# Performance work log

Measured on AMD Instinct MI355X. Metric: run time of the kernel, lower is better.

## Reference

```python
import jax, jax.numpy as jnp
import numpy as np

N_NODES = 100000


def gcn_conv(x, edge_index, W, b, n_nodes):
    """PyG GCNConv: add self-loops, symmetric deg norm, linear, scatter-add, bias."""
    self_loops = jnp.arange(n_nodes, dtype=edge_index.dtype)
    src = jnp.concatenate([edge_index[0], self_loops])  # [E+N]
    dst = jnp.concatenate([edge_index[1], self_loops])  # [E+N]
    xw = x @ W  # [N, out]
    deg = jax.ops.segment_sum(jnp.ones_like(dst, dtype=xw.dtype), dst, num_segments=n_nodes)
    deg_inv_sqrt = jnp.where(deg > 0, jax.lax.rsqrt(deg), 0.0)
    norm = deg_inv_sqrt[src] * deg_inv_sqrt[dst]  # [E+N]
    msg = xw[src] * norm[:, None]                 # [E+N, out]
    out = jax.ops.segment_sum(msg, dst, num_segments=n_nodes)
    return out + b


def setup_inputs() -> dict:
    key = jax.random.key(0)
    ks = jax.random.split(key, 8)
    n, e, d_in, h = N_NODES, 3200000, 128, 16
    x = jax.random.normal(ks[0], (n, d_in), dtype=jnp.float32)
    edge_index = jax.random.randint(ks[1], (2, e), 0, n, dtype=jnp.int64)
    W1 = jax.random.normal(ks[2], (d_in, h), dtype=jnp.float32) / np.sqrt(d_in)
    b1 = jnp.zeros((h,), dtype=jnp.float32)
    W2 = jax.random.normal(ks[3], (h, h), dtype=jnp.float32) / np.sqrt(h)
    b2 = jnp.zeros((h,), dtype=jnp.float32)
    W_lin = jax.random.normal(ks[4], (h, 1), dtype=jnp.float32) / np.sqrt(h)
    b_lin = jnp.zeros((1,), dtype=jnp.float32)
    return {"x": x, "edge_index": edge_index, "W1": W1, "b1": b1,
            "W2": W2, "b2": b2, "W_lin": W_lin, "b_lin": b_lin}


def reference(x, edge_index, W1, b1, W2, b2, W_lin, b_lin):
    n = x.shape[0]
    h = gcn_conv(x, edge_index, W1, b1, n)
    h = jax.nn.relu(h)
    # dropout is identity in eval mode (training=False)
    h = gcn_conv(h, edge_index, W2, b2, n)
    h = jax.nn.relu(h)
    out = h @ W_lin + b_lin  # [N, 1]
    return out.squeeze(-1)   # [N]
```

## Files before the change

### kernel.cpp

```cpp
#include <hip/hip_runtime.h>
#include <hip/hip_fp16.h>

#define DIN 128
#define HDIM 16
#define NB 512
#define BDIV_MAX 256
#define CAPB 7168
#define HSTR 17
#define BIN_EPT 16
#define TPB 512
#define BINSZ (TPB * BIN_EPT)
#define FXS 65536.0f
#define FXI (1.0f / 65536.0f)

__device__ __forceinline__ float4 f4add(float4 a, float4 b) {
    return make_float4(a.x + b.x, a.y + b.y, a.z + b.z, a.w + b.w);
}

__device__ __forceinline__ float4 h4_to_f4(uint2 u) {
    __half2 a = *(__half2*)&u.x, b = *(__half2*)&u.y;
    float2 fa = __half22float2(a), fb = __half22float2(b);
    return make_float4(fa.x, fa.y, fb.x, fb.y);
}
__device__ __forceinline__ uint2 f4_to_h4(float4 v) {
    __half2 a = __floats2half2_rn(v.x, v.y);
    __half2 b = __floats2half2_rn(v.z, v.w);
    uint2 u;
    u.x = *(unsigned*)&a;
    u.y = *(unsigned*)&b;
    return u;
}

__device__ __forceinline__ int load_idx(const void* ei, long long i, int is64) {
    return is64 ? (int)((const long long*)ei)[i] : ((const int*)ei)[i];
}

__device__ __forceinline__ void fx_acc(int* a, float4 v) {
    atomicAdd(a + 0, __float2int_rn(v.x * FXS));
    atomicAdd(a + 1, __float2int_rn(v.y * FXS));
    atomicAdd(a + 2, __float2int_rn(v.z * FXS));
    atomicAdd(a + 3, __float2int_rn(v.w * FXS));
}

__global__ __launch_bounds__(512) void k_main(const void* __restrict__ ei, long long E,
                                              int bdiv, unsigned Mdiv,
                                              int* __restrict__ bcur,
                                              unsigned int* __restrict__ recs,
                                              const float* __restrict__ x,
                                              const float* __restrict__ W1,
                                              unsigned int* __restrict__ y1,
                                              int n, int nbin) {
    __shared__ int cnt[NB];
    __shared__ int base[NB];
    __shared__ float Ws[DIN * HDIM];
    int tid = threadIdx.x;
    if ((int)blockIdx.x < nbin) {
        unsigned probe = ((const unsigned*)ei)[1 + 2 * (tid & 63)];
        int is64 = (__ballot(probe != 0) == 0ull) ? 1 : 0;
        cnt[tid] = 0;
        __syncthreads();
        long long e0 = (long long)blockIdx.x * BINSZ;
        int s[BIN_EPT], dl[BIN_EPT], b[BIN_EPT];
        if (e0 + BINSZ <= E) {
            int d[BIN_EPT];
            if (is64) {
                const longlong2* ps = (const longlong2*)((const long long*)ei + e0);
                const longlong2* pd = (const longlong2*)((const long long*)ei + E + e0);
#pragma unroll
                for (int i = 0; i < BIN_EPT / 2; i++) {
                    longlong2 vs = ps[i * TPB + tid];
                    longlong2 vd = pd[i * TPB + tid];
                    s[2 * i + 0] = (int)vs.x; s[2 * i + 1] = (int)vs.y;
                    d[2 * i + 0] = (int)vd.x; d[2 * i + 1] = (int)vd.y;
                }
            } else {
                const int4* ps = (const int4*)((const int*)ei + e0);
                const int4* pd = (const int4*)((const int*)ei + E + e0);
#pragma unroll
                for (int i = 0; i < BIN_EPT / 4; i++) {
                    int4 vs = ps[i * TPB + tid];
                    int4 vd = pd[i * TPB + tid];
                    s[4 * i + 0] = vs.x; s[4 * i + 1] = vs.y;
                    s[4 * i + 2] = vs.z; s[4 * i + 3] = vs.w;
                    d[4 * i + 0] = vd.x; d[4 * i + 1] = vd.y;
                    d[4 * i + 2] = vd.z; d[4 * i + 3] = vd.w;
                }
            }
#pragma unroll
            for (int i = 0; i < BIN_EPT; i++) {
                int bb = Mdiv ? (int)__umulhi((unsigned)d[i], Mdiv) : d[i];
                b[i] = bb;
                dl[i] = d[i] - bb * bdiv;
                atomicAdd(&cnt[bb], 1);
            }
        } else {
#pragma unroll
            for (int i = 0; i < BIN_EPT; i++) {
                long long e = e0 + (long long)i * TPB + tid;
                if (e < E) {
                    s[i] = load_idx(ei, e, is64);
                    int d = load_idx(ei, E + e, is64);
                    int bb = Mdiv ? (int)__umulhi((unsigned)d, Mdiv) : d;
                    b[i] = bb;
                    dl[i] = d - bb * bdiv;
                    atomicAdd(&cnt[bb], 1);
                } else {
                    b[i] = -1;
                }
            }
        }
        __syncthreads();
        base[tid] = atomicAdd(&bcur[tid], cnt[tid]);
        cnt[tid] = 0;
        __syncthreads();
#pragma unroll
        for (int i = 0; i < BIN_EPT; i++) {
            if (b[i] >= 0) {
                int off = atomicAdd(&cnt[b[i]], 1);
                int pos = base[b[i]] + off;
                if (pos < CAPB) {
                    recs[(size_t)b[i] * CAPB + pos] =
                        ((unsigned)dl[i] << 18) | (unsigned)s[i];
                }
            }
        }
    } else {
        for (int i = tid; i < DIN * HDIM; i += TPB) Ws[i] = W1[i];
        __syncthreads();
        int node = ((int)blockIdx.x - nbin) * TPB + tid;
        if (node >= n) return;
        uint2* yr = (uint2*)(y1 + (size_t)node * 8);
        float acc[HDIM];
#pragma unroll
        for (int f = 0; f < HDIM; f++) acc[f] = 0.f;
        const float4* xr = (const float4*)(x + (size_t)node * DIN);
#pragma unroll 8
        for (int k4 = 0; k4 < DIN / 4; k4++) {
            float4 xv = xr[k4];
            int k = k4 * 4;
#pragma unroll
            for (int f = 0; f < HDIM; f++) {
                acc[f] += xv.x * Ws[(k + 0) * HDIM + f];
                acc[f] += xv.y * Ws[(k + 1) * HDIM + f];
                acc[f] += xv.z * Ws[(k + 2) * HDIM + f];
                acc[f] += xv.w * Ws[(k + 3) * HDIM + f];
            }
        }
#pragma unroll
        for (int q = 0; q < 4; q++)
            yr[q] = f4_to_h4(make_float4(acc[q * 4 + 0], acc[q * 4 + 1],
                                         acc[q * 4 + 2], acc[q * 4 + 3]));
    }
}

__global__ __launch_bounds__(512) void k_deg(const unsigned int* __restrict__ recs,
                                             const int* __restrict__ bcur,
                                             float* __restrict__ dis,
                                             unsigned int* __restrict__ y1,
                                             int n, int bdiv) {
    __shared__ int cnt[BDIV_MAX];
    int tid = threadIdx.x, b = blockIdx.x;
    if (tid < BDIV_MAX) cnt[tid] = 0;
    __syncthreads();
    int lo = b * bdiv; if (lo > n) lo = n;
    int hi = lo + bdiv; if (hi > n) hi = n;
    int nd = hi - lo;
    int m = bcur[b]; if (m > CAPB) m = CAPB;
    const unsigned int* r = recs + (size_t)b * CAPB;
    for (int i = tid; i < m; i += 512)
        atomicAdd(&cnt[r[i] >> 18], 1);
    __syncthreads();
    int q = tid & 3, g = tid >> 2;
    uint2* yv = (uint2*)y1;
    for (int j = g; j < nd; j += 128) {
        int node = lo + j;
        float dv = rsqrtf((float)cnt[j] + 1.0f);
        if (q == 0) dis[node] = dv;
        float4 t = h4_to_f4(yv[(size_t)node * 4 + q]);
        yv[(size_t)node * 4 + q] =
            f4_to_h4(make_float4(t.x * dv, t.y * dv, t.z * dv, t.w * dv));
    }
}

__global__ __launch_bounds__(512) void k_agg1(const unsigned int* __restrict__ recs,
                                              const int* __restrict__ bcur,
                                              const float* __restrict__ dis,
                                              const unsigned int* __restrict__ y1,
                                              const float* __restrict__ b1,
                                              const float* __restrict__ W2,
                                              unsigned int* __restrict__ y2,
                                              int n, int bdiv) {
    __shared__ int acc[BDIV_MAX * HSTR];
    __shared__ unsigned int sh[CAPB];
    __shared__ float4 Ws4[HDIM][4];
    int tid = threadIdx.x, b = blockIdx.x;
    if (tid < HDIM * 4)
        ((float4*)Ws4)[tid] = ((const float4*)W2)[tid];
    int lo = b * bdiv; if (lo > n) lo = n;
    int hi = lo + bdiv; if (hi > n) hi = n;
    int nd = hi - lo;
    for (int i = tid; i < bdiv * HSTR; i += 512) acc[i] = 0;
    int m = bcur[b]; if (m > CAPB) m = CAPB;
    const uint4* r4 = (const uint4*)(recs + (size_t)b * CAPB);
    int m4 = (m + 3) >> 2;
    for (int k = tid; k < m4; k += 512) ((uint4*)sh)[k] = r4[k];
    __syncthreads();
    const uint2* yv = (const uint2*)y1;
    int q = tid & 3, g = tid >> 2;
    int i = g;
    for (; i + 384 < m; i += 512) {
        unsigned r0 = sh[i], r1 = sh[i + 128], r2 = sh[i + 256], r3 = sh[i + 384];
        float4 v0 = h4_to_f4(yv[(size_t)(r0 & 0x3FFFFu) * 4 + q]);
        float4 v1 = h4_to_f4(yv[(size_t)(r1 & 0x3FFFFu) * 4 + q]);
        float4 v2 = h4_to_f4(yv[(size_t)(r2 & 0x3FFFFu) * 4 + q]);
        float4 v3 = h4_to_f4(yv[(size_t)(r3 & 0x3FFFFu) * 4 + q]);
        fx_acc(&acc[(r0 >> 18) * HSTR + q * 4], v0);
        fx_acc(&acc[(r1 >> 18) * HSTR + q * 4], v1);
        fx_acc(&acc[(r2 >> 18) * HSTR + q * 4], v2);
        fx_acc(&acc[(r3 >> 18) * HSTR + q * 4], v3);
    }
    for (; i < m; i += 128) {
        unsigned r0 = sh[i];
        float4 v0 = h4_to_f4(yv[(size_t)(r0 & 0x3FFFFu) * 4 + q]);
        fx_acc(&acc[(r0 >> 18) * HSTR + q * 4], v0);
    }
    __syncthreads();
    float4 bb = ((const float4*)b1)[q];
    for (int j = g; j < nd; j += 128) {
        int node = lo + j;
        float dv = dis[node];
        int* ap = &acc[j * HSTR + q * 4];
        float4 a = make_float4((float)ap[0] * FXI, (float)ap[1] * FXI,
                               (float)ap[2] * FXI, (float)ap[3] * FXI);
        a = f4add(a, h4_to_f4(yv[(size_t)node * 4 + q]));
        float4 h;
        h.x = fmaxf(dv * a.x + bb.x, 0.f);
        h.y = fmaxf(dv * a.y + bb.y, 0.f);
        h.z = fmaxf(dv * a.z + bb.z, 0.f);
        h.w = fmaxf(dv * a.w + bb.w, 0.f);
        float4 o = make_float4(0.f, 0.f, 0.f, 0.f);
#pragma unroll
        for (int k = 0; k < 4; k++) {
            float4 hk;
            hk.x = __shfl(h.x, k, 4); hk.y = __shfl(h.y, k, 4);
            hk.z = __shfl(h.z, k, 4); hk.w = __shfl(h.w, k, 4);
            float hv[4] = {hk.x, hk.y, hk.z, hk.w};
#pragma unroll
            for (int c = 0; c < 4; c++) {
                float4 w = Ws4[k * 4 + c][q];
                o.x += hv[c] * w.x; o.y += hv[c] * w.y;
                o.z += hv[c] * w.z; o.w += hv[c] * w.w;
            }
        }
        ((uint2*)y2)[(size_t)node * 4 + q] =
            f4_to_h4(make_float4(o.x * dv, o.y * dv, o.z * dv, o.w * dv));
    }
}

__global__ __launch_bounds__(512) void k_agg2(const unsigned int* __restrict__ recs,
                                              const int* __restrict__ bcur,
                                              const float* __restrict__ dis,
                                              const unsigned int* __restrict__ y2,
                                              const float* __restrict__ b2,
                                              const float* __restrict__ Wlin,
                                              const float* __restrict__ blin,
                                              float* __restrict__ out,
                                              int n, int bdiv) {
    __shared__ int acc[BDIV_MAX * HSTR];
    __shared__ unsigned int sh[CAPB];
    int tid = threadIdx.x, b = blockIdx.x;
    int lo = b * bdiv; if (lo > n) lo = n;
    int hi = lo + bdiv; if (hi > n) hi = n;
    int nd = hi - lo;
    for (int i = tid; i < bdiv * HSTR; i += 512) acc[i] = 0;
    int m = bcur[b]; if (m > CAPB) m = CAPB;
    const uint4* r4 = (const uint4*)(recs + (size_t)b * CAPB);
    int m4 = (m + 3) >> 2;
    for (int k = tid; k < m4; k += 512) ((uint4*)sh)[k] = r4[k];
    __syncthreads();
    const uint2* yv = (const uint2*)y2;
    int q = tid & 3, g = tid >> 2;
    int i = g;
    for (; i + 384 < m; i += 512) {
        unsigned r0 = sh[i], r1 = sh[i + 128], r2 = sh[i + 256], r3 = sh[i + 384];
        float4 v0 = h4_to_f4(yv[(size_t)(r0 & 0x3FFFFu) * 4 + q]);
        float4 v1 = h4_to_f4(yv[(size_t)(r1 & 0x3FFFFu) * 4 + q]);
        float4 v2 = h4_to_f4(yv[(size_t)(r2 & 0x3FFFFu) * 4 + q]);
        float4 v3 = h4_to_f4(yv[(size_t)(r3 & 0x3FFFFu) * 4 + q]);
        fx_acc(&acc[(r0 >> 18) * HSTR + q * 4], v0);
        fx_acc(&acc[(r1 >> 18) * HSTR + q * 4], v1);
        fx_acc(&acc[(r2 >> 18) * HSTR + q * 4], v2);
        fx_acc(&acc[(r3 >> 18) * HSTR + q * 4], v3);
    }
    for (; i < m; i += 128) {
        unsigned r0 = sh[i];
        float4 v0 = h4_to_f4(yv[(size_t)(r0 & 0x3FFFFu) * 4 + q]);
        fx_acc(&acc[(r0 >> 18) * HSTR + q * 4], v0);
    }
    __syncthreads();
    float4 bb = ((const float4*)b2)[q];
    float4 wl = ((const float4*)Wlin)[q];
    for (int j = g; j < nd; j += 128) {
        int node = lo + j;
        float dv = dis[node];
        int* ap = &acc[j * HSTR + q * 4];
        float4 a = make_float4((float)ap[0] * FXI, (float)ap[1] * FXI,
                               (float)ap[2] * FXI, (float)ap[3] * FXI);
        a = f4add(a, h4_to_f4(yv[(size_t)node * 4 + q]));
        float v = 0.f;
        v += fmaxf(dv * a.x + bb.x, 0.f) * wl.x;
        v += fmaxf(dv * a.y + bb.y, 0.f) * wl.y;
        v += fmaxf(dv * a.z + bb.z, 0.f) * wl.z;
        v += fmaxf(dv * a.w + bb.w, 0.f) * wl.w;
        v += __shfl_xor(v, 1, 4);
        v += __shfl_xor(v, 2, 4);
        if (q == 0) out[node] = v + blin[0];
    }
}

extern "C" void kernel_launch(void* const* d_in, const int* in_sizes, int n_in,
                              void* d_out, int out_size, void* d_ws, size_t ws_size,
                              hipStream_t stream) {
    const float* x    = (const float*)d_in[0];
    const void*  ei   = d_in[1];
    const float* W1   = (const float*)d_in[2];
    const float* b1   = (const float*)d_in[3];
    const float* W2   = (const float*)d_in[4];
    const float* b2   = (const float*)d_in[5];
    const float* Wlin = (const float*)d_in[6];
    const float* blin = (const float*)d_in[7];
    float* out = (float*)d_out;

    const int n = in_sizes[0] / DIN;
    const long long E = in_sizes[1] / 2;
    const int bdiv = (n + NB - 1) / NB;
    const unsigned Mdiv = (bdiv > 1)
        ? (unsigned)(((1ull << 32) + (unsigned)bdiv - 1) / (unsigned)bdiv) : 0u;

    char* ws = (char*)d_ws;
    size_t off = 0;
    auto alloc = [&](size_t bytes) { char* p = ws + off; off += (bytes + 255) & ~(size_t)255; return p; };
    int*   bcur = (int*)alloc(NB * 4);
    float* dis  = (float*)alloc((size_t)n * 4);
    unsigned int* y1 = (unsigned int*)alloc((size_t)n * 8 * 4);
    unsigned int* y2 = (unsigned int*)alloc((size_t)n * 8 * 4);
    unsigned int* recs = (unsigned int*)alloc((size_t)NB * CAPB * 4);

    const int nb_xw  = (n + TPB - 1) / TPB;
    const int nb_bin = (int)((E + BINSZ - 1) / BINSZ);

    hipMemsetAsync(bcur, 0, NB * sizeof(int), stream);
    k_main<<<nb_bin + nb_xw, TPB, 0, stream>>>(ei, E, bdiv, Mdiv, bcur, recs, x, W1, y1, n, nb_bin);
    k_deg<<<NB, 512, 0, stream>>>(recs, bcur, dis, y1, n, bdiv);
    k_agg1<<<NB, 512, 0, stream>>>(recs, bcur, dis, y1, b1, W2, y2, n, bdiv);
    k_agg2<<<NB, 512, 0, stream>>>(recs, bcur, dis, y2, b2, Wlin, blin, out, n, bdiv);
}
```

Before: 184.9 us.

## Replace shared-memory atomic scatter with per-block counting sort and register gather

Both aggregation kernels now counting-sort each bin's edge records by destination inside shared memory, padding every node's list to a multiple of four with a dummy zero row at index n. Each node then gathers its neighbours' half-precision features into registers, with no fixed-point LDS atomics. This targets the cost of four integer atomics per edge per thread. In exchange it adds a 512-wide prefix scan, a second pass over the records, a padding fill, and an extra zeroed feature row. Degree is recomputed from the sorted counts, so the precomputed dis array is no longer read.

After: 194.7 us. 1.05x slower.

```diff
diff --git a/kernel.cpp b/kernel.cpp
--- a/kernel.cpp
+++ b/kernel.cpp
@@ -6,12 +6,10 @@
 #define NB 512
 #define BDIV_MAX 256
 #define CAPB 7168
-#define HSTR 17
+#define CAPP 7936
 #define BIN_EPT 16
 #define TPB 512
 #define BINSZ (TPB * BIN_EPT)
-#define FXS 65536.0f
-#define FXI (1.0f / 65536.0f)
 
 __device__ __forceinline__ float4 f4add(float4 a, float4 b) {
     return make_float4(a.x + b.x, a.y + b.y, a.z + b.z, a.w + b.w);
@@ -33,13 +31,6 @@
 
 __device__ __forceinline__ int load_idx(const void* ei, long long i, int is64) {
     return is64 ? (int)((const long long*)ei)[i] : ((const int*)ei)[i];
-}
-
-__device__ __forceinline__ void fx_acc(int* a, float4 v) {
-    atomicAdd(a + 0, __float2int_rn(v.x * FXS));
-    atomicAdd(a + 1, __float2int_rn(v.y * FXS));
-    atomicAdd(a + 2, __float2int_rn(v.z * FXS));
-    atomicAdd(a + 3, __float2int_rn(v.w * FXS));
 }
 
 __global__ __launch_bounds__(512) void k_main(const void* __restrict__ ei, long long E,
@@ -128,8 +119,14 @@
         for (int i = tid; i < DIN * HDIM; i += TPB) Ws[i] = W1[i];
         __syncthreads();
         int node = ((int)blockIdx.x - nbin) * TPB + tid;
-        if (node >= n) return;
+        if (node > n) return;
         uint2* yr = (uint2*)(y1 + (size_t)node * 8);
+        if (node == n) {
+            uint2 z; z.x = 0u; z.y = 0u;
+#pragma unroll
+            for (int q = 0; q < 4; q++) yr[q] = z;
+            return;
+        }
         float acc[HDIM];
 #pragma unroll
         for (int f = 0; f < HDIM; f++) acc[f] = 0.f;
@@ -182,72 +179,107 @@
     }
 }
 
-__global__ __launch_bounds__(512) void k_agg1(const unsigned int* __restrict__ recs,
-                                              const int* __restrict__ bcur,
-                                              const float* __restrict__ dis,
-                                              const unsigned int* __restrict__ y1,
-                                              const float* __restrict__ b1,
-                                              const float* __restrict__ W2,
-                                              unsigned int* __restrict__ y2,
-                                              int n, int bdiv) {
-    __shared__ int acc[BDIV_MAX * HSTR];
-    __shared__ unsigned int sh[CAPB];
+__global__ __launch_bounds__(512) void k_sg1(const unsigned int* __restrict__ recs,
+                                             const int* __restrict__ bcur,
+                                             const unsigned int* __restrict__ y1,
+                                             const float* __restrict__ b1,
+                                             const float* __restrict__ W2,
+                                             unsigned int* __restrict__ y2,
+                                             int n, int bdiv) {
+    __shared__ int cnt_sh[BDIV_MAX];
+    __shared__ int sc[512];
+    __shared__ int stx[BDIV_MAX];
+    __shared__ int dgx[BDIV_MAX];
+    __shared__ unsigned int ord[CAPP];
     __shared__ float4 Ws4[HDIM][4];
     int tid = threadIdx.x, b = blockIdx.x;
     if (tid < HDIM * 4)
         ((float4*)Ws4)[tid] = ((const float4*)W2)[tid];
+    if (b == 0 && tid < 4) {
+        uint2 z; z.x = 0u; z.y = 0u;
+        ((uint2*)y2)[(size_t)n * 4 + tid] = z;
+    }
     int lo = b * bdiv; if (lo > n) lo = n;
     int hi = lo + bdiv; if (hi > n) hi = n;
     int nd = hi - lo;
-    for (int i = tid; i < bdiv * HSTR; i += 512) acc[i] = 0;
+    if (tid < BDIV_MAX) cnt_sh[tid] = 0;
+    __syncthreads();
     int m = bcur[b]; if (m > CAPB) m = CAPB;
-    const uint4* r4 = (const uint4*)(recs + (size_t)b * CAPB);
-    int m4 = (m + 3) >> 2;
-    for (int k = tid; k < m4; k += 512) ((uint4*)sh)[k] = r4[k];
-    __syncthreads();
+    const unsigned int* r = recs + (size_t)b * CAPB;
+    for (int i = tid; i < m; i += 512)
+        atomicAdd(&cnt_sh[r[i] >> 18], 1);
+    __syncthreads();
+    int v  = (tid < nd) ? cnt_sh[tid] : 0;
+    int pv = (v + 3) & ~3;
+    sc[tid] = pv;
+    __syncthreads();
+    for (int off = 1; off < 512; off <<= 1) {
+        int t = (tid >= off) ? sc[tid - off] : 0;
+        __syncthreads();
+        sc[tid] += t;
+        __syncthreads();
+    }
+    int ptot = sc[511];
+    if (ptot > CAPP) ptot = CAPP;
+    if (tid < nd) {
+        int excl = sc[tid] - pv;
+        stx[tid] = excl; dgx[tid] = v;
+        cnt_sh[tid] = excl;
+    }
+    for (int i = tid; i < ptot; i += 512) ord[i] = (unsigned)n;
+    __syncthreads();
+    for (int i = tid; i < m; i += 512) {
+        unsigned rv = r[i];
+        int pos = atomicAdd(&cnt_sh[rv >> 18], 1);
+        if (pos < CAPP) ord[pos] = rv & 0x3FFFFu;
+    }
+    __syncthreads();
+    int q = tid & 3, g = tid >> 2;
     const uint2* yv = (const uint2*)y1;
-    int q = tid & 3, g = tid >> 2;
-    int i = g;
-    for (; i + 384 < m; i += 512) {
-        unsigned r0 = sh[i], r1 = sh[i + 128], r2 = sh[i + 256], r3 = sh[i + 384];
-        float4 v0 = h4_to_f4(yv[(size_t)(r0 & 0x3FFFFu) * 4 + q]);
-        float4 v1 = h4_to_f4(yv[(size_t)(r1 & 0x3FFFFu) * 4 + q]);
-        float4 v2 = h4_to_f4(yv[(size_t)(r2 & 0x3FFFFu) * 4 + q]);
-        float4 v3 = h4_to_f4(yv[(size_t)(r3 & 0x3FFFFu) * 4 + q]);
-        fx_acc(&acc[(r0 >> 18) * HSTR + q * 4], v0);
-        fx_acc(&acc[(r1 >> 18) * HSTR + q * 4], v1);
-        fx_acc(&acc[(r2 >> 18) * HSTR + q * 4], v2);
-        fx_acc(&acc[(r3 >> 18) * HSTR + q * 4], v3);
-    }
-    for (; i < m; i += 128) {
-        unsigned r0 = sh[i];
-        float4 v0 = h4_to_f4(yv[(size_t)(r0 & 0x3FFFFu) * 4 + q]);
-        fx_acc(&acc[(r0 >> 18) * HSTR + q * 4], v0);
-    }
-    __syncthreads();
     float4 bb = ((const float4*)b1)[q];
     for (int j = g; j < nd; j += 128) {
         int node = lo + j;
-        float dv = dis[node];
-        int* ap = &acc[j * HSTR + q * 4];
-        float4 a = make_float4((float)ap[0] * FXI, (float)ap[1] * FXI,
-                               (float)ap[2] * FXI, (float)ap[3] * FXI);
-        a = f4add(a, h4_to_f4(yv[(size_t)node * 4 + q]));
+        int st = stx[j], dg = dgx[j];
+        int pe = st + ((dg + 3) & ~3);
+        float4 a0 = make_float4(0.f, 0.f, 0.f, 0.f), a1 = a0, a2 = a0, a3 = a0;
+        int k = st;
+        for (; k + 8 <= pe; k += 8) {
+            int4 c0 = *(const int4*)&ord[k];
+            int4 c1 = *(const int4*)&ord[k + 4];
+            uint2 v0 = yv[(size_t)c0.x * 4 + q], v1 = yv[(size_t)c0.y * 4 + q];
+            uint2 v2 = yv[(size_t)c0.z * 4 + q], v3 = yv[(size_t)c0.w * 4 + q];
+            uint2 v4 = yv[(size_t)c1.x * 4 + q], v5 = yv[(size_t)c1.y * 4 + q];
+            uint2 v6 = yv[(size_t)c1.z * 4 + q], v7 = yv[(size_t)c1.w * 4 + q];
+            a0 = f4add(a0, h4_to_f4(v0)); a1 = f4add(a1, h4_to_f4(v1));
+            a2 = f4add(a2, h4_to_f4(v2)); a3 = f4add(a3, h4_to_f4(v3));
+            a0 = f4add(a0, h4_to_f4(v4)); a1 = f4add(a1, h4_to_f4(v5));
+            a2 = f4add(a2, h4_to_f4(v6)); a3 = f4add(a3, h4_to_f4(v7));
+        }
+        for (; k < pe; k += 4) {
+            int4 c0 = *(const int4*)&ord[k];
+            uint2 v0 = yv[(size_t)c0.x * 4 + q], v1 = yv[(size_t)c0.y * 4 + q];
+            uint2 v2 = yv[(size_t)c0.z * 4 + q], v3 = yv[(size_t)c0.w * 4 + q];
+            a0 = f4add(a0, h4_to_f4(v0)); a1 = f4add(a1, h4_to_f4(v1));
+            a2 = f4add(a2, h4_to_f4(v2)); a3 = f4add(a3, h4_to_f4(v3));
+        }
+        float4 acc = f4add(f4add(a0, a1), f4add(a2, a3));
+        acc = f4add(acc, h4_to_f4(yv[(size_t)node * 4 + q]));
+        float dv = rsqrtf((float)dg + 1.0f);
         float4 h;
-        h.x = fmaxf(dv * a.x + bb.x, 0.f);
-        h.y = fmaxf(dv * a.y + bb.y, 0.f);
-        h.z = fmaxf(dv * a.z + bb.z, 0.f);
-        h.w = fmaxf(dv * a.w + bb.w, 0.f);
+        h.x = fmaxf(dv * acc.x + bb.x, 0.f);
+        h.y = fmaxf(dv * acc.y + bb.y, 0.f);
+        h.z = fmaxf(dv * acc.z + bb.z, 0.f);
+        h.w = fmaxf(dv * acc.w + bb.w, 0.f);
         float4 o = make_float4(0.f, 0.f, 0.f, 0.f);
 #pragma unroll
-        for (int k = 0; k < 4; k++) {
+        for (int kk = 0; kk < 4; kk++) {
             float4 hk;
-            hk.x = __shfl(h.x, k, 4); hk.y = __shfl(h.y, k, 4);
-            hk.z = __shfl(h.z, k, 4); hk.w = __shfl(h.w, k, 4);
+            hk.x = __shfl(h.x, kk, 4); hk.y = __shfl(h.y, kk, 4);
+            hk.z = __shfl(h.z, kk, 4); hk.w = __shfl(h.w, kk, 4);
             float hv[4] = {hk.x, hk.y, hk.z, hk.w};
 #pragma unroll
             for (int c = 0; c < 4; c++) {
-                float4 w = Ws4[k * 4 + c][q];
+                float4 w = Ws4[kk * 4 + c][q];
                 o.x += hv[c] * w.x; o.y += hv[c] * w.y;
                 o.z += hv[c] * w.z; o.w += hv[c] * w.w;
             }
@@ -257,64 +289,95 @@
     }
 }
 
-__global__ __launch_bounds__(512) void k_agg2(const unsigned int* __restrict__ recs,
-                                              const int* __restrict__ bcur,
-                                              const float* __restrict__ dis,
-                                              const unsigned int* __restrict__ y2,
-                                              const float* __restrict__ b2,
-                                              const float* __restrict__ Wlin,
-                                              const float* __restrict__ blin,
-                                              float* __restrict__ out,
-                                              int n, int bdiv) {
-    __shared__ int acc[BDIV_MAX * HSTR];
-    __shared__ unsigned int sh[CAPB];
+__global__ __launch_bounds__(512) void k_sg2(const unsigned int* __restrict__ recs,
+                                             const int* __restrict__ bcur,
+                                             const unsigned int* __restrict__ y2,
+                                             const float* __restrict__ b2,
+                                             const float* __restrict__ Wlin,
+                                             const float* __restrict__ blin,
+                                             float* __restrict__ out,
+                                             int n, int bdiv) {
+    __shared__ int cnt_sh[BDIV_MAX];
+    __shared__ int sc[512];
+    __shared__ int stx[BDIV_MAX];
+    __shared__ int dgx[BDIV_MAX];
+    __shared__ unsigned int ord[CAPP];
     int tid = threadIdx.x, b = blockIdx.x;
     int lo = b * bdiv; if (lo > n) lo = n;
     int hi = lo + bdiv; if (hi > n) hi = n;
     int nd = hi - lo;
-    for (int i = tid; i < bdiv * HSTR; i += 512) acc[i] = 0;
+    if (tid < BDIV_MAX) cnt_sh[tid] = 0;
+    __syncthreads();
     int m = bcur[b]; if (m > CAPB) m = CAPB;
-    const uint4* r4 = (const uint4*)(recs + (size_t)b * CAPB);
-    int m4 = (m + 3) >> 2;
-    for (int k = tid; k < m4; k += 512) ((uint4*)sh)[k] = r4[k];
-    __syncthreads();
+    const unsigned int* r = recs + (size_t)b * CAPB;
+    for (int i = tid; i < m; i += 512)
+        atomicAdd(&cnt_sh[r[i] >> 18], 1);
+    __syncthreads();
+    int v  = (tid < nd) ? cnt_sh[tid] : 0;
+    int pv = (v + 3) & ~3;
+    sc[tid] = pv;
+    __syncthreads();
+    for (int off = 1; off < 512; off <<= 1) {
+        int t = (tid >= off) ? sc[tid - off] : 0;
+        __syncthreads();
+        sc[tid] += t;
+        __syncthreads();
+    }
+    int ptot = sc[511];
+    if (ptot > CAPP) ptot = CAPP;
+    if (tid < nd) {
+        int excl = sc[tid] - pv;
+        stx[tid] = excl; dgx[tid] = v;
+        cnt_sh[tid] = excl;
+    }
+    for (int i = tid; i < ptot; i += 512) ord[i] = (unsigned)n;
+    __syncthreads();
+    for (int i = tid; i < m; i += 512) {
+        unsigned rv = r[i];
+        int pos = atomicAdd(&cnt_sh[rv >> 18], 1);
+        if (pos < CAPP) ord[pos] = rv & 0x3FFFFu;
+    }
+    __syncthreads();
+    int q = tid & 3, g = tid >> 2;
     const uint2* yv = (const uint2*)y2;
-    int q = tid & 3, g = tid >> 2;
-    int i = g;
-    for (; i + 384 < m; i += 512) {
-        unsigned r0 = sh[i], r1 = sh[i + 128], r2 = sh[i + 256], r3 = sh[i + 384];
-        float4 v0 = h4_to_f4(yv[(size_t)(r0 & 0x3FFFFu) * 4 + q]);
-        float4 v1 = h4_to_f4(yv[(size_t)(r1 & 0x3FFFFu) * 4 + q]);
-        float4 v2 = h4_to_f4(yv[(size_t)(r2 & 0x3FFFFu) * 4 + q]);
-        float4 v3 = h4_to_f4(yv[(size_t)(r3 & 0x3FFFFu) * 4 + q]);
-        fx_acc(&acc[(r0 >> 18) * HSTR + q * 4], v0);
-        fx_acc(&acc[(r1 >> 18) * HSTR + q * 4], v1);
-        fx_acc(&acc[(r2 >> 18) * HSTR + q * 4], v2);
-        fx_acc(&acc[(r3 >> 18) * HSTR + q * 4], v3);
-    }
-    for (; i < m; i += 128) {
-        unsigned r0 = sh[i];
-        float4 v0 = h4_to_f4(yv[(size_t)(r0 & 0x3FFFFu) * 4 + q]);
-        fx_acc(&acc[(r0 >> 18) * HSTR + q * 4], v0);
-    }
-    __syncthreads();
     float4 bb = ((const float4*)b2)[q];
     float4 wl = ((const float4*)Wlin)[q];
     for (int j = g; j < nd; j += 128) {
         int node = lo + j;
-        float dv = dis[node];
-        int* ap = &acc[j * HSTR + q * 4];
-        float4 a = make_float4((float)ap[0] * FXI, (float)ap[1] * FXI,
-                               (float)ap[2] * FXI, (float)ap[3] * FXI);
-        a = f4add(a, h4_to_f4(yv[(size_t)node * 4 + q]));
-        float v = 0.f;
-        v += fmaxf(dv * a.x + bb.x, 0.f) * wl.x;
-        v += fmaxf(dv * a.y + bb.y, 0.f) * wl.y;
-        v += fmaxf(dv * a.z + bb.z, 0.f) * wl.z;
-        v += fmaxf(dv * a.w + bb.w, 0.f) * wl.w;
-        v += __shfl_xor(v, 1, 4);
-        v += __shfl_xor(v, 2, 4);
-        if (q == 0) out[node] = v + blin[0];
+        int st = stx[j], dg = dgx[j];
+        int pe = st + ((dg + 3) & ~3);
+        float4 a0 = make_float4(0.f, 0.f, 0.f, 0.f), a1 = a0, a2 = a0, a3 = a0;
+        int k = st;
+        for (; k + 8 <= pe; k += 8) {
+            int4 c0 = *(const int4*)&ord[k];
+            int4 c1 = *(const int4*)&ord[k + 4];
+            uint2 v0 = yv[(size_t)c0.x * 4 + q], v1 = yv[(size_t)c0.y * 4 + q];
+            uint2 v2 = yv[(size_t)c0.z * 4 + q], v3 = yv[(size_t)c0.w * 4 + q];
+            uint2 v4 = yv[(size_t)c1.x * 4 + q], v5 = yv[(size_t)c1.y * 4 + q];
+            uint2 v6 = yv[(size_t)c1.z * 4 + q], v7 = yv[(size_t)c1.w * 4 + q];
+            a0 = f4add(a0, h4_to_f4(v0)); a1 = f4add(a1, h4_to_f4(v1));
+            a2 = f4add(a2, h4_to_f4(v2)); a3 = f4add(a3, h4_to_f4(v3));
+            a0 = f4add(a0, h4_to_f4(v4)); a1 = f4add(a1, h4_to_f4(v5));
+            a2 = f4add(a2, h4_to_f4(v6)); a3 = f4add(a3, h4_to_f4(v7));
+        }
+        for (; k < pe; k += 4) {
+            int4 c0 = *(const int4*)&ord[k];
+            uint2 v0 = yv[(size_t)c0.x * 4 + q], v1 = yv[(size_t)c0.y * 4 + q];
+            uint2 v2 = yv[(size_t)c0.z * 4 + q], v3 = yv[(size_t)c0.w * 4 + q];
+            a0 = f4add(a0, h4_to_f4(v0)); a1 = f4add(a1, h4_to_f4(v1));
+            a2 = f4add(a2, h4_to_f4(v2)); a3 = f4add(a3, h4_to_f4(v3));
+        }
+        float4 acc = f4add(f4add(a0, a1), f4add(a2, a3));
+        acc = f4add(acc, h4_to_f4(yv[(size_t)node * 4 + q]));
+        float dv = rsqrtf((float)dg + 1.0f);
+        float vv = 0.f;
+        vv += fmaxf(dv * acc.x + bb.x, 0.f) * wl.x;
+        vv += fmaxf(dv * acc.y + bb.y, 0.f) * wl.y;
+        vv += fmaxf(dv * acc.z + bb.z, 0.f) * wl.z;
+        vv += fmaxf(dv * acc.w + bb.w, 0.f) * wl.w;
+        vv += __shfl_xor(vv, 1, 4);
+        vv += __shfl_xor(vv, 2, 4);
+        if (q == 0) out[node] = vv + blin[0];
     }
 }
 
@@ -342,16 +405,16 @@
     auto alloc = [&](size_t bytes) { char* p = ws + off; off += (bytes + 255) & ~(size_t)255; return p; };
     int*   bcur = (int*)alloc(NB * 4);
     float* dis  = (float*)alloc((size_t)n * 4);
-    unsigned int* y1 = (unsigned int*)alloc((size_t)n * 8 * 4);
-    unsigned int* y2 = (unsigned int*)alloc((size_t)n * 8 * 4);
+    unsigned int* y1 = (unsigned int*)alloc((size_t)(n + 1) * 8 * 4);
+    unsigned int* y2 = (unsigned int*)alloc((size_t)(n + 1) * 8 * 4);
     unsigned int* recs = (unsigned int*)alloc((size_t)NB * CAPB * 4);
 
-    const int nb_xw  = (n + TPB - 1) / TPB;
+    const int nb_xw  = (n + 1 + TPB - 1) / TPB;
     const int nb_bin = (int)((E + BINSZ - 1) / BINSZ);
 
     hipMemsetAsync(bcur, 0, NB * sizeof(int), stream);
     k_main<<<nb_bin + nb_xw, TPB, 0, stream>>>(ei, E, bdiv, Mdiv, bcur, recs, x, W1, y1, n, nb_bin);
     k_deg<<<NB, 512, 0, stream>>>(recs, bcur, dis, y1, n, bdiv);
-    k_agg1<<<NB, 512, 0, stream>>>(recs, bcur, dis, y1, b1, W2, y2, n, bdiv);
-    k_agg2<<<NB, 512, 0, stream>>>(recs, bcur, dis, y2, b2, Wlin, blin, out, n, bdiv);
-}
+    k_sg1<<<NB, 512, 0, stream>>>(recs, bcur, y1, b1, W2, y2, n, bdiv);
+    k_sg2<<<NB, 512, 0, stream>>>(recs, bcur, y2, b2, Wlin, blin, out, n, bdiv);
+}
```
